# Kernel tuning notes

Measured on AMD Instinct MI355X. Metric: run time of the kernel, lower is better.

The kernel has to match this reference:

```python
import jax, jax.numpy as jnp
import numpy as np
import math

B, S, D_MODEL, N_HEADS = 4, 2048, 1024, 16
D_HEAD = D_MODEL // N_HEADS

def _xavier(key, shape, gain):
    # nn.init.xavier_uniform_ on [n_heads, fan_in, fan_out]: fan from last two dims
    fan_in, fan_out = shape[-2], shape[-1]
    bound = gain * math.sqrt(6.0 / (fan_in + fan_out))
    return jax.random.uniform(key, shape, jnp.float32, -bound, bound)

def setup_inputs() -> dict:
    key = jax.random.key(0)
    ks = jax.random.split(key, 5)
    g = 1.0 / math.sqrt(2.0)
    return {
        "x": jax.random.normal(ks[0], (B, S, D_MODEL), jnp.float32),
        "W_Q": _xavier(ks[1], (N_HEADS, D_MODEL, D_HEAD), g),
        "W_K": _xavier(ks[2], (N_HEADS, D_MODEL, D_HEAD), g),
        "W_V": _xavier(ks[3], (N_HEADS, D_MODEL, D_HEAD), g),
        "W_O": _xavier(ks[4], (N_HEADS, D_HEAD, D_MODEL), 1.0),
        "b_Q": jnp.zeros((N_HEADS, D_HEAD), jnp.float32),
        "b_K": jnp.zeros((N_HEADS, D_HEAD), jnp.float32),
        "b_V": jnp.zeros((N_HEADS, D_HEAD), jnp.float32),
        "b_O": jnp.zeros((D_MODEL,), jnp.float32),
    }

def reference(x, W_Q, W_K, W_V, W_O, b_Q, b_K, b_V, b_O):
    # q,k,v: [b, s, h, d_head]
    q = jnp.einsum('bsd,hde->bshe', x, W_Q) + b_Q
    k = jnp.einsum('bsd,hde->bshe', x, W_K) + b_K
    v = jnp.einsum('bsd,hde->bshe', x, W_V) + b_V
    scores = jnp.einsum('bqhe,bkhe->bhqk', q, k) / jnp.sqrt(jnp.float32(D_HEAD))
    attn = jax.nn.softmax(scores, axis=-1)  # [b, h, q, k]
    v_out = jnp.einsum('bkhe,bhqk->bqhe', v, attn)
    return jnp.einsum('bqhe,hed->bqd', v_out, W_O) + b_O
```

## Files before the change

### kernel.cpp

```cpp
#include <hip/hip_runtime.h>
#include <hip/hip_bf16.h>
#include <cmath>

#define B_ 4
#define S_ 2048
#define DM_ 1024
#define H_ 16
#define DH_ 64
#define BS_ (B_*S_)

typedef __bf16 bf16x8 __attribute__((ext_vector_type(8)));
typedef __bf16 bf16x4 __attribute__((ext_vector_type(4)));
typedef float  floatx4 __attribute__((ext_vector_type(4)));

__device__ __forceinline__ void gl_lds16(const __bf16* g, __bf16* l) {
  __builtin_amdgcn_global_load_lds(
      (const __attribute__((address_space(1))) void*)g,
      (__attribute__((address_space(3))) void*)l, 16, 0, 0);
}

__global__ void transpose_kernel(const float* __restrict__ src, __bf16* __restrict__ dst,
                                 int R, int C, long srcBatch, long dstBatch) {
  __shared__ __bf16 tile[32][33];
  int b = blockIdx.z;
  long sb = (long)b * srcBatch;
  dst += (long)b * dstBatch;
  int c0 = blockIdx.x * 32, r0 = blockIdx.y * 32;
  int tx = threadIdx.x, ty = threadIdx.y;
  #pragma unroll
  for (int i = 0; i < 32; i += 8)
    tile[ty + i][tx] = (__bf16)src[sb + (long)(r0 + ty + i) * C + (c0 + tx)];
  __syncthreads();
  #pragma unroll
  for (int i = 0; i < 32; i += 8)
    dst[(long)(c0 + ty + i) * R + (r0 + tx)] = tile[tx][ty + i];
}

__global__ void cvt_kernel(const float* __restrict__ src, __bf16* __restrict__ dst) {
  long i = ((long)blockIdx.x * 256 + threadIdx.x) * 8;
  float4 a = *(const float4*)(src + i);
  float4 b = *(const float4*)(src + i + 4);
  bf16x8 t;
  t[0] = (__bf16)a.x; t[1] = (__bf16)a.y; t[2] = (__bf16)a.z; t[3] = (__bf16)a.w;
  t[4] = (__bf16)b.x; t[5] = (__bf16)b.y; t[6] = (__bf16)b.z; t[7] = (__bf16)b.w;
  *(bf16x8*)(dst + i) = t;
}

#define BM 128
#define BN 128
#define BK 64

template<int EPI>
__global__ __launch_bounds__(256, 4) void gemm_kernel(
    const __bf16* __restrict__ A, const __bf16* __restrict__ Bt,
    int M, int N, int K,
    const float* __restrict__ bq, const float* __restrict__ bk,
    const float* __restrict__ bv, const float* __restrict__ bo,
    __bf16* __restrict__ q_ws, __bf16* __restrict__ k_ws,
    __bf16* __restrict__ vT_ws, float* __restrict__ out) {

  __shared__ __align__(16) __bf16 smem[17408];
  __bf16* As = smem;
  __bf16* Bs = smem + 8192;

  int tid  = threadIdx.x;
  int wave = tid >> 6, lane = tid & 63;
  int quad = lane >> 4, l15 = lane & 15;
  int wm = (wave >> 1) * 64, wn = (wave & 1) * 64;

  int nbx = gridDim.x;
  int lid = blockIdx.y * nbx + blockIdx.x;
  int cpx = (nbx * gridDim.y) >> 3;
  int sid = (lid & 7) * cpx + (lid >> 3);
  long m0 = (long)(sid / nbx) * BM;
  long n0 = (long)(sid % nbx) * BN;

  floatx4 acc[4][4] = {};

  int r  = tid >> 3, c8 = tid & 7;
  int cx = c8 ^ (r & 7);
  const __bf16* Asrc = A  + (m0 + r) * (long)K + cx * 8;
  const __bf16* Bsrc = Bt + (n0 + r) * (long)K + cx * 8;

#define STAGE(k0) do {                                                       \
    _Pragma("unroll")                                                        \
    for (int i = 0; i < 4; i++) {                                            \
      gl_lds16(Asrc + (long)(i * 32) * K + (k0), &As[(i * 256 + tid) * 8]);  \
      gl_lds16(Bsrc + (long)(i * 32) * K + (k0), &Bs[(i * 256 + tid) * 8]);  \
    }                                                                        \
  } while (0)

  int swz = l15 & 7;
  const int NT = K / BK;

  STAGE(0);

  for (int t = 0; t < NT; ++t) {
    __syncthreads();

    #pragma unroll
    for (int kk = 0; kk < 2; kk++) {
      bf16x8 af[4], bff[4];
      #pragma unroll
      for (int mt = 0; mt < 4; mt++)
        af[mt] = *(const bf16x8*)(&As[(wm + mt * 16 + l15) * 64 + (((kk * 4 + quad) ^ swz) * 8)]);
      #pragma unroll
      for (int nt = 0; nt < 4; nt++)
        bff[nt] = *(const bf16x8*)(&Bs[(wn + nt * 16 + l15) * 64 + (((kk * 4 + quad) ^ swz) * 8)]);
      #pragma unroll
      for (int mt = 0; mt < 4; mt++)
        #pragma unroll
        for (int nt = 0; nt < 4; nt++)
          acc[mt][nt] = __builtin_amdgcn_mfma_f32_16x16x32_bf16(af[mt], bff[nt], acc[mt][nt], 0, 0, 0);
    }

    if (t + 1 < NT) {
      __syncthreads();
      STAGE((t + 1) * BK);
    }
  }
#undef STAGE

  if (EPI == 0) {
    int seg = (int)(n0 >> 10);
    if (seg < 2) {
      #pragma unroll
      for (int nt = 0; nt < 4; nt++) {
        long n = n0 + wn + nt * 16 + l15;
        int he  = (int)(n & 1023);
        int h = he >> 6, e = he & 63;
        const float* bias = (seg == 0 ? bq : bk);
        float bval = bias[he];
        float scale = (seg == 0 ? 0.125f * 1.44269504088896340f : 1.0f);
        __bf16* dst0 = (seg == 0 ? q_ws : k_ws);
        #pragma unroll
        for (int mt = 0; mt < 4; mt++) {
          #pragma unroll
          for (int rr = 0; rr < 4; rr++) {
            long m = m0 + wm + mt * 16 + quad * 4 + rr;
            int b = (int)(m >> 11), s = (int)(m & 2047);
            float v = (acc[mt][nt][rr] + bval) * scale;
            dst0[((long)(b * 16 + h) * 2048 + s) * 64 + e] = (__bf16)v;
          }
        }
      }
    } else {
      __syncthreads();
      __bf16* vl = smem + wave * 4352;
      #pragma unroll
      for (int nt = 0; nt < 4; nt++) {
        long n = n0 + wn + nt * 16 + l15;
        float bval = bv[(int)(n & 1023)];
        #pragma unroll
        for (int mt = 0; mt < 4; mt++) {
          bf16x4 pw;
          #pragma unroll
          for (int rr = 0; rr < 4; rr++) pw[rr] = (__bf16)(acc[mt][nt][rr] + bval);
          *(bf16x4*)(&vl[(nt * 16 + l15) * 68 + mt * 16 + quad * 4]) = pw;
        }
      }
      asm volatile("s_waitcnt lgkmcnt(0)" ::: "memory");
      int bb = (int)((m0 + wm) >> 11), s0 = (int)((m0 + wm) & 2047);
      #pragma unroll
      for (int rep = 0; rep < 2; rep++) {
        int j = (lane >> 1) + rep * 32;
        long n = n0 + wn + j;
        int he = (int)(n & 1023);
        int h = he >> 6, e = he & 63;
        __bf16* dst = vT_ws + ((long)(bb * 16 + h) * 64 + e) * 2048 + s0 + (lane & 1) * 32;
        const __bf16* srcl = &vl[j * 68 + (lane & 1) * 32];
        #pragma unroll
        for (int c = 0; c < 4; c++)
          *(bf16x8*)(dst + c * 8) = *(const bf16x8*)(srcl + c * 8);
      }
    }
  } else {
    #pragma unroll
    for (int mt = 0; mt < 4; mt++) {
      #pragma unroll
      for (int rr = 0; rr < 4; rr++) {
        long m = m0 + wm + mt * 16 + quad * 4 + rr;
        #pragma unroll
        for (int nt = 0; nt < 4; nt++) {
          long n = n0 + wn + nt * 16 + l15;
          out[m * N + n] = acc[mt][nt][rr] + bo[n];
        }
      }
    }
  }
}

#define KBLK 64

__global__ __launch_bounds__(256, 4) void attn_kernel(
    const __bf16* __restrict__ Q, const __bf16* __restrict__ Kk,
    const __bf16* __restrict__ Vt, __bf16* __restrict__ vout) {

  __shared__ __align__(16) __bf16 Kb[2][64 * 64];
  __shared__ __align__(16) __bf16 Vb[2][64 * 64];
  __shared__ __align__(16) __bf16 Pb[4][16 * 64];

  int tid = threadIdx.x, wave = tid >> 6, lane = tid & 63;
  int quad = lane >> 4, l15 = lane & 15;

  int id = blockIdx.x;
  int xcd = id & 7, rest = id >> 3;
  int qt = rest & 15, bhhi = rest >> 4;
  int bh = bhhi * 8 + xcd;
  int b = bh >> 4, h = bh & 15;
  int q0 = qt * 128 + wave * 32;

  const __bf16* Qbh = Q  + (long)(b * 16 + h) * 2048 * 64;
  const __bf16* Kbh = Kk + (long)(b * 16 + h) * 2048 * 64;
  const __bf16* Vbh = Vt + (long)(b * 16 + h) * 64 * 2048;

  int rs0 = tid >> 3, cc0 = tid & 7;
  int ccs = cc0 ^ (rs0 & 7);
  const __bf16* Ksrc0 = Kbh + (long)rs0 * 64 + ccs * 8;
  const __bf16* Ksrc1 = Kbh + (long)(rs0 + 32) * 64 + ccs * 8;
  const __bf16* Vsrc0 = Vbh + (long)rs0 * 2048 + ccs * 8;
  const __bf16* Vsrc1 = Vbh + (long)(rs0 + 32) * 2048 + ccs * 8;

#define STAGE(buf, kb) do {                                   \
    gl_lds16(Ksrc0 + (long)(kb) * 64, &Kb[buf][tid * 8]);      \
    gl_lds16(Ksrc1 + (long)(kb) * 64, &Kb[buf][tid * 8 + 2048]); \
    gl_lds16(Vsrc0 + (kb),            &Vb[buf][tid * 8]);      \
    gl_lds16(Vsrc1 + (kb),            &Vb[buf][tid * 8 + 2048]); \
  } while (0)

  bf16x8 qf[2][2];
  #pragma unroll
  for (int qh = 0; qh < 2; qh++)
    #pragma unroll
    for (int t = 0; t < 2; t++)
      qf[qh][t] = *(const bf16x8*)(Qbh + (long)(q0 + qh * 16 + l15) * 64 + t * 32 + quad * 8);

  floatx4 o[2][4] = {};
  floatx4 ol[2] = {};
  bf16x8 onesv;
  #pragma unroll
  for (int j = 0; j < 8; j++) onesv[j] = (__bf16)1.0f;

  int swz = l15 & 7;

  STAGE(0, 0);

  for (int kb = 0; kb < 2048; kb += KBLK) {
    int cur = (kb >> 6) & 1;

    __syncthreads();
    if (kb + KBLK < 2048) STAGE(cur ^ 1, kb + KBLK);

    floatx4 sc[2][4];
    __builtin_amdgcn_s_setprio(1);
    #pragma unroll
    for (int nt = 0; nt < 4; nt++) {
      const __bf16* kp = &Kb[cur][(nt * 16 + l15) * 64];
      bf16x8 k0 = *(const bf16x8*)(kp + ((0 + quad) ^ swz) * 8);
      bf16x8 k1 = *(const bf16x8*)(kp + ((4 + quad) ^ swz) * 8);
      #pragma unroll
      for (int qh = 0; qh < 2; qh++) {
        floatx4 z = { 0.f, 0.f, 0.f, 0.f };
        z = __builtin_amdgcn_mfma_f32_16x16x32_bf16(k0, qf[qh][0], z, 0, 0, 0);
        sc[qh][nt] = __builtin_amdgcn_mfma_f32_16x16x32_bf16(k1, qf[qh][1], z, 0, 0, 0);
      }
    }
    __builtin_amdgcn_s_setprio(0);

    #pragma unroll
    for (int qh = 0; qh < 2; qh++) {
      #pragma unroll
      for (int nt = 0; nt < 4; nt++) {
        bf16x4 pw;
        #pragma unroll
        for (int rr = 0; rr < 4; rr++)
          pw[rr] = (__bf16)__builtin_amdgcn_exp2f(sc[qh][nt][rr]);
        *(bf16x4*)(&Pb[wave][l15 * 64 + (((nt * 2 + (quad >> 1)) ^ swz) * 8) + (quad & 1) * 4]) = pw;
      }

      __builtin_amdgcn_s_setprio(1);
      #pragma unroll
      for (int t = 0; t < 2; t++) {
        bf16x8 pf = *(const bf16x8*)(&Pb[wave][l15 * 64 + ((t * 4 + quad) ^ swz) * 8]);
        ol[qh] = __builtin_amdgcn_mfma_f32_16x16x32_bf16(onesv, pf, ol[qh], 0, 0, 0);
        #pragma unroll
        for (int dn = 0; dn < 4; dn++) {
          bf16x8 vf = *(const bf16x8*)(&Vb[cur][(dn * 16 + l15) * 64 + ((t * 4 + quad) ^ swz) * 8]);
          o[qh][dn] = __builtin_amdgcn_mfma_f32_16x16x32_bf16(vf, pf, o[qh][dn], 0, 0, 0);
        }
      }
      __builtin_amdgcn_s_setprio(0);
    }
  }
#undef STAGE

  #pragma unroll
  for (int qh = 0; qh < 2; qh++) {
    float rl = 1.f / ol[qh][0];
    int s = q0 + qh * 16 + l15;
    __bf16* outr = vout + ((long)(b * 2048 + s) * 16 + h) * 64;
    #pragma unroll
    for (int dn = 0; dn < 4; dn++) {
      bf16x4 w;
      #pragma unroll
      for (int rr = 0; rr < 4; rr++) w[rr] = (__bf16)(o[qh][dn][rr] * rl);
      *(bf16x4*)(outr + dn * 16 + quad * 4) = w;
    }
  }
}

extern "C" void kernel_launch(void* const* d_in, const int* in_sizes, int n_in,
                              void* d_out, int out_size, void* d_ws, size_t ws_size,
                              hipStream_t stream) {
  const float* x  = (const float*)d_in[0];
  const float* WQ = (const float*)d_in[1];
  const float* WK = (const float*)d_in[2];
  const float* WV = (const float*)d_in[3];
  const float* WO = (const float*)d_in[4];
  const float* bq = (const float*)d_in[5];
  const float* bk = (const float*)d_in[6];
  const float* bv = (const float*)d_in[7];
  const float* bo = (const float*)d_in[8];
  float* out = (float*)d_out;

  uint8_t* ws = (uint8_t*)d_ws;
  const long MB16 = 16777216;
  __bf16* q_ws  = (__bf16*)(ws);
  __bf16* k_ws  = (__bf16*)(ws + 1 * MB16);
  __bf16* vT_ws = (__bf16*)(ws + 2 * MB16);
  __bf16* Wt    = (__bf16*)(ws + 3 * MB16);
  __bf16* vout  = (__bf16*)(ws + 3 * MB16);
  __bf16* WOt   = (__bf16*)(ws);
  __bf16* xb    = (__bf16*)d_out;

  dim3 tb(32, 8);
  transpose_kernel<<<dim3(2, 32, 16), tb, 0, stream>>>(WQ, Wt,               1024, 64, 65536, 65536);
  transpose_kernel<<<dim3(2, 32, 16), tb, 0, stream>>>(WK, Wt + 1024 * 1024, 1024, 64, 65536, 65536);
  transpose_kernel<<<dim3(2, 32, 16), tb, 0, stream>>>(WV, Wt + 2048 * 1024, 1024, 64, 65536, 65536);

  cvt_kernel<<<dim3(4096), 256, 0, stream>>>(x, xb);

  gemm_kernel<0><<<dim3(3072 / BN, 8192 / BM), 256, 0, stream>>>(
      xb, Wt, BS_, 3072, DM_, bq, bk, bv, nullptr, q_ws, k_ws, vT_ws, nullptr);

  attn_kernel<<<dim3(1024), 256, 0, stream>>>(q_ws, k_ws, vT_ws, vout);

  transpose_kernel<<<dim3(32, 32, 1), tb, 0, stream>>>(WO, WOt, 1024, 1024, 0, 0);

  gemm_kernel<1><<<dim3(1024 / BN, 8192 / BM), 256, 0, stream>>>(
      vout, WOt, BS_, DM_, DM_, nullptr, nullptr, nullptr, bo, nullptr, nullptr, nullptr, out);
}
```

Before: 267.7 us.

## Load V fragments directly from global, merge QKV transposes, batch PV MFMAs

The attention kernel no longer stages V tiles through LDS. Each lane now reads its V fragments straight from global memory into registers, and P for both query halves is written to a double-sized LDS buffer so the PV MFMAs for both halves run in one interleaved loop. The three weight-transpose launches are merged into a single launch. This cuts LDS traffic and capacity and removes two kernel launches, but it trades async LDS prefetch for global loads that are not prefetched and may stall the MFMA loop, and it raises register pressure.

Measured after the change: 377.1 us. 40.9% more time.

```diff
diff --git a/kernel.cpp b/kernel.cpp
--- a/kernel.cpp
+++ b/kernel.cpp
@@ -34,6 +34,26 @@
   #pragma unroll
   for (int i = 0; i < 32; i += 8)
     dst[(long)(c0 + ty + i) * R + (r0 + tx)] = tile[tx][ty + i];
+}
+
+__global__ void transpose_qkv_kernel(const float* __restrict__ WQ,
+                                     const float* __restrict__ WK,
+                                     const float* __restrict__ WV,
+                                     __bf16* __restrict__ dst) {
+  __shared__ __bf16 tile[32][33];
+  int z = blockIdx.z;
+  int mat = z >> 4, head = z & 15;
+  const float* src = (mat == 0 ? WQ : (mat == 1 ? WK : WV)) + (long)head * 65536;
+  dst += (long)mat * 1048576 + (long)head * 65536;
+  int c0 = blockIdx.x * 32, r0 = blockIdx.y * 32;
+  int tx = threadIdx.x, ty = threadIdx.y;
+  #pragma unroll
+  for (int i = 0; i < 32; i += 8)
+    tile[ty + i][tx] = (__bf16)src[(long)(r0 + ty + i) * 64 + (c0 + tx)];
+  __syncthreads();
+  #pragma unroll
+  for (int i = 0; i < 32; i += 8)
+    dst[(long)(c0 + ty + i) * 1024 + (r0 + tx)] = tile[tx][ty + i];
 }
 
 __global__ void cvt_kernel(const float* __restrict__ src, __bf16* __restrict__ dst) {
@@ -197,8 +217,7 @@
     const __bf16* __restrict__ Vt, __bf16* __restrict__ vout) {
 
   __shared__ __align__(16) __bf16 Kb[2][64 * 64];
-  __shared__ __align__(16) __bf16 Vb[2][64 * 64];
-  __shared__ __align__(16) __bf16 Pb[4][16 * 64];
+  __shared__ __align__(16) __bf16 Pb[4][2][16 * 64];
 
   int tid = threadIdx.x, wave = tid >> 6, lane = tid & 63;
   int quad = lane >> 4, l15 = lane & 15;
@@ -218,14 +237,10 @@
   int ccs = cc0 ^ (rs0 & 7);
   const __bf16* Ksrc0 = Kbh + (long)rs0 * 64 + ccs * 8;
   const __bf16* Ksrc1 = Kbh + (long)(rs0 + 32) * 64 + ccs * 8;
-  const __bf16* Vsrc0 = Vbh + (long)rs0 * 2048 + ccs * 8;
-  const __bf16* Vsrc1 = Vbh + (long)(rs0 + 32) * 2048 + ccs * 8;
-
-#define STAGE(buf, kb) do {                                   \
-    gl_lds16(Ksrc0 + (long)(kb) * 64, &Kb[buf][tid * 8]);      \
+
+#define STAGE(buf, kb) do {                                      \
+    gl_lds16(Ksrc0 + (long)(kb) * 64, &Kb[buf][tid * 8]);        \
     gl_lds16(Ksrc1 + (long)(kb) * 64, &Kb[buf][tid * 8 + 2048]); \
-    gl_lds16(Vsrc0 + (kb),            &Vb[buf][tid * 8]);      \
-    gl_lds16(Vsrc1 + (kb),            &Vb[buf][tid * 8 + 2048]); \
   } while (0)
 
   bf16x8 qf[2][2];
@@ -242,6 +257,7 @@
   for (int j = 0; j < 8; j++) onesv[j] = (__bf16)1.0f;
 
   int swz = l15 & 7;
+  const __bf16* Vl = Vbh + (long)l15 * 2048 + quad * 8;
 
   STAGE(0, 0);
 
@@ -267,6 +283,13 @@
     }
     __builtin_amdgcn_s_setprio(0);
 
+    bf16x8 vf[2][4];
+    #pragma unroll
+    for (int t = 0; t < 2; t++)
+      #pragma unroll
+      for (int dn = 0; dn < 4; dn++)
+        vf[t][dn] = *(const bf16x8*)(Vl + (long)(dn * 16) * 2048 + kb + t * 32);
+
     #pragma unroll
     for (int qh = 0; qh < 2; qh++) {
       #pragma unroll
@@ -275,22 +298,24 @@
         #pragma unroll
         for (int rr = 0; rr < 4; rr++)
           pw[rr] = (__bf16)__builtin_amdgcn_exp2f(sc[qh][nt][rr]);
-        *(bf16x4*)(&Pb[wave][l15 * 64 + (((nt * 2 + (quad >> 1)) ^ swz) * 8) + (quad & 1) * 4]) = pw;
-      }
-
-      __builtin_amdgcn_s_setprio(1);
-      #pragma unroll
-      for (int t = 0; t < 2; t++) {
-        bf16x8 pf = *(const bf16x8*)(&Pb[wave][l15 * 64 + ((t * 4 + quad) ^ swz) * 8]);
-        ol[qh] = __builtin_amdgcn_mfma_f32_16x16x32_bf16(onesv, pf, ol[qh], 0, 0, 0);
-        #pragma unroll
-        for (int dn = 0; dn < 4; dn++) {
-          bf16x8 vf = *(const bf16x8*)(&Vb[cur][(dn * 16 + l15) * 64 + ((t * 4 + quad) ^ swz) * 8]);
-          o[qh][dn] = __builtin_amdgcn_mfma_f32_16x16x32_bf16(vf, pf, o[qh][dn], 0, 0, 0);
-        }
-      }
-      __builtin_amdgcn_s_setprio(0);
-    }
+        *(bf16x4*)(&Pb[wave][qh][l15 * 64 + (((nt * 2 + (quad >> 1)) ^ swz) * 8) + (quad & 1) * 4]) = pw;
+      }
+    }
+
+    __builtin_amdgcn_s_setprio(1);
+    #pragma unroll
+    for (int t = 0; t < 2; t++) {
+      bf16x8 pf0 = *(const bf16x8*)(&Pb[wave][0][l15 * 64 + ((t * 4 + quad) ^ swz) * 8]);
+      bf16x8 pf1 = *(const bf16x8*)(&Pb[wave][1][l15 * 64 + ((t * 4 + quad) ^ swz) * 8]);
+      ol[0] = __builtin_amdgcn_mfma_f32_16x16x32_bf16(onesv, pf0, ol[0], 0, 0, 0);
+      ol[1] = __builtin_amdgcn_mfma_f32_16x16x32_bf16(onesv, pf1, ol[1], 0, 0, 0);
+      #pragma unroll
+      for (int dn = 0; dn < 4; dn++) {
+        o[0][dn] = __builtin_amdgcn_mfma_f32_16x16x32_bf16(vf[t][dn], pf0, o[0][dn], 0, 0, 0);
+        o[1][dn] = __builtin_amdgcn_mfma_f32_16x16x32_bf16(vf[t][dn], pf1, o[1][dn], 0, 0, 0);
+      }
+    }
+    __builtin_amdgcn_s_setprio(0);
   }
 #undef STAGE
 
@@ -334,9 +359,7 @@
   __bf16* xb    = (__bf16*)d_out;
 
   dim3 tb(32, 8);
-  transpose_kernel<<<dim3(2, 32, 16), tb, 0, stream>>>(WQ, Wt,               1024, 64, 65536, 65536);
-  transpose_kernel<<<dim3(2, 32, 16), tb, 0, stream>>>(WK, Wt + 1024 * 1024, 1024, 64, 65536, 65536);
-  transpose_kernel<<<dim3(2, 32, 16), tb, 0, stream>>>(WV, Wt + 2048 * 1024, 1024, 64, 65536, 65536);
+  transpose_qkv_kernel<<<dim3(2, 32, 48), tb, 0, stream>>>(WQ, WK, WV, Wt);
 
   cvt_kernel<<<dim3(4096), 256, 0, stream>>>(x, xb);
 
```
